# Optimization experiments

Measured on AMD Instinct MI355X. Metric: run time of the kernel, lower is better.

The kernel has to match this reference:

```python
import jax, jax.numpy as jnp
import numpy as np

B, N, I, O, H = 4, 2047, 256, 128, 4
NEG = -1e18
SLOPE = 0.2


def setup_inputs() -> dict:
    key = jax.random.key(0)
    ks = jax.random.split(key, 8)
    x = jax.random.normal(ks[0], (B, N, I), dtype=jnp.float32)
    prior_feature = jax.random.normal(ks[1], (B, O), dtype=jnp.float32)
    x_mask = jax.random.randint(ks[2], (B, N + 1), 0, 2).astype(bool)
    # learned parameters (xavier-ish scaling)
    W_lin = jax.random.normal(ks[3], (O, I), dtype=jnp.float32) * (1.0 / np.sqrt(I))
    w_head = jax.random.normal(ks[4], (H, O, O), dtype=jnp.float32) * (1.0 / np.sqrt(O))
    a_src = jax.random.normal(ks[5], (H, O), dtype=jnp.float32) * (1.0 / np.sqrt(O))
    a_dst = jax.random.normal(ks[6], (H, O), dtype=jnp.float32) * (1.0 / np.sqrt(O))
    bias = jnp.zeros((O,), dtype=jnp.float32)
    return {"x": x, "prior_feature": prior_feature, "x_mask": x_mask,
            "W_lin": W_lin, "w_head": w_head, "a_src": a_src, "a_dst": a_dst, "bias": bias}


def reference(x, prior_feature, x_mask, W_lin, w_head, a_src, a_dst, bias):
    # self_linear (no bias), then concat prior feature as extra node -> [B, N1, O]
    h = jnp.einsum('bni,oi->bno', x, W_lin)
    hp = jnp.concatenate([h, prior_feature[:, None, :]], axis=1)  # [B, N1, O]
    # per-head projection: [B,1,N1,O] @ [H,O,O] -> [B,H,N1,O]
    hp = jnp.einsum('bno,hop->bhnp', hp, w_head)
    t = jnp.tanh(hp)
    s_src = jnp.einsum('bhno,ho->bhn', t, a_src)  # [B,H,N1]
    s_dst = jnp.einsum('bhno,ho->bhn', t, a_dst)  # [B,H,N1]
    attn = s_src[..., :, None] + s_dst[..., None, :]  # [B,H,N1,N1]
    attn = jnp.where(attn >= 0, attn, SLOPE * attn)  # leaky_relu(0.2)
    mask = x_mask[:, :, None] | x_mask[:, None, :]    # [B,N1,N1]
    attn = jnp.where(mask[:, None, :, :], jnp.float32(NEG), attn)
    attn = jax.nn.softmax(attn, axis=-1)
    # dropout p=0.0 -> identity
    out = jnp.einsum('bhij,bhjo->bhio', attn, hp) + bias  # [B,H,N1,O]
    return out.mean(axis=1)  # mean over heads -> [B,N1,O]
```

## Files before the change

### kernel.cpp

```cpp
#include <hip/hip_runtime.h>
#include <hip/hip_bf16.h>
#include <cmath>


#define B_ 4
#define N_ 2047
#define N1 2048
#define I_ 256
#define O_ 128
#define H_ 4
#define NBINS 512
#define NCHUNK 4
#define CBINS (NBINS / NCHUNK)
#define STR 132
#define SLOPEC 0.2f
#define HS_STR 136
#define XS_STR 72

typedef unsigned short u16;
typedef unsigned char u8;
typedef short bf16x8 __attribute__((ext_vector_type(8)));
typedef float f32x4 __attribute__((ext_vector_type(4)));
#define MFMA16(a,b,c) __builtin_amdgcn_mfma_f32_16x16x32_bf16(a,b,c,0,0,0)

__device__ __forceinline__ float bf2f(u16 v){
  union { unsigned u; float f; } x; x.u = ((unsigned)v) << 16; return x.f;
}
__device__ __forceinline__ u16 f2bf(float f){
  union { float f; unsigned u; } x; x.f = f;
  unsigned u = x.u;
  return (u16)((u + 0x7FFFu + ((u >> 16) & 1u)) >> 16);
}
__device__ __forceinline__ float ldv(const void* p, int bf, size_t i){
  if (bf) return bf2f(reinterpret_cast<const u16*>(p)[i]);
  return reinterpret_cast<const float*>(p)[i];
}
__device__ __forceinline__ void ld8(const void* p, int bf, size_t i, float* o){
  if (bf){
    uint4 v = *reinterpret_cast<const uint4*>(reinterpret_cast<const u16*>(p) + i);
    o[0]=bf2f((u16)(v.x&0xFFFF)); o[1]=bf2f((u16)(v.x>>16));
    o[2]=bf2f((u16)(v.y&0xFFFF)); o[3]=bf2f((u16)(v.y>>16));
    o[4]=bf2f((u16)(v.z&0xFFFF)); o[5]=bf2f((u16)(v.z>>16));
    o[6]=bf2f((u16)(v.w&0xFFFF)); o[7]=bf2f((u16)(v.w>>16));
  } else {
    const float4* q = reinterpret_cast<const float4*>(reinterpret_cast<const float*>(p) + i);
    float4 a = q[0], b = q[1];
    o[0]=a.x; o[1]=a.y; o[2]=a.z; o[3]=a.w;
    o[4]=b.x; o[5]=b.y; o[6]=b.z; o[7]=b.w;
  }
}
__device__ __forceinline__ void st8bf(u16* dst, const void* src, int bf, size_t i){
  if (bf){
    *reinterpret_cast<uint4*>(dst) =
      *reinterpret_cast<const uint4*>(reinterpret_cast<const u16*>(src) + i);
  } else {
    float v[8]; ld8(src, 0, i, v);
    u16 tmp[8];
#pragma unroll
    for (int m = 0; m < 8; m++) tmp[m] = f2bf(v[m]);
    *reinterpret_cast<uint4*>(dst) = *reinterpret_cast<uint4*>(tmp);
  }
}
__device__ __forceinline__ float clS(float v){ return fminf(30.f, fmaxf(-30.f, v)); }
__device__ __forceinline__ float clH(float v){ return fminf(1e4f, fmaxf(-1e4f, v)); }
__device__ __forceinline__ int binOf(float v, float lo, float inv){
  int c = (int)((v - lo) * inv);
  c = c < 0 ? 0 : c;
  c = c > NBINS - 1 ? NBINS - 1 : c;
  return c;
}
__device__ __forceinline__ int rdmask(const u8* m, int mode, int idx){
  return mode ? (m[idx] != 0) : (((const int*)m)[idx] != 0);
}

__global__ __launch_bounds__(1024) void k0_detect(const u8* __restrict__ mask,
                                                  const void* x, const void* prior,
                                                  const void* Wlin, const void* wh,
                                                  const void* asr, const void* ads,
                                                  int* __restrict__ flags,
                                                  float* __restrict__ colsum){
  __shared__ int c[8];
  const int t = threadIdx.x;
  for (int i = t; i < B_ * H_ * O_; i += 1024) colsum[i] = 0.f;
  if (t < 8) c[t] = 0;
  __syncthreads();
  int local = 0;
  for (int i = t; i < B_ * N1; i += 1024)
    if ((i & 3) && mask[i]) local = 1;
  if (local) atomicOr(&c[0], 1);
  const void* ptrs[6] = {x, prior, Wlin, wh, asr, ads};
  const int   lens[6] = {4096, 512, 4096, 4096, 512, 512};
  for (int k = 0; k < 6; k++){
    const u16* p = (const u16*)ptrs[k];
    int g = 0;
    for (int i = t; i < lens[k]; i += 1024){
      int e = (p[i] >> 7) & 0xFF;
      if (e >= 0xC0) g++;
    }
    if (g) atomicAdd(&c[k + 1], g);
  }
  __syncthreads();
  if (t == 0) flags[0] = c[0];
  else if (t <= 6) flags[t] = (c[t] < 4) ? 1 : 0;
}

__global__ __launch_bounds__(256) void ktr(const void* __restrict__ w_head,
                                           const int* __restrict__ flags,
                                           u16* __restrict__ wT){
  const int fw = flags[4];
  const int idx = blockIdx.x * 256 + threadIdx.x;
  const int h = idx >> 14, rem = idx & 16383, p = rem >> 7, o = rem & 127;
  wT[idx] = f2bf(ldv(w_head, fw, ((size_t)h * O_ + o) * O_ + p));
}

__global__ __launch_bounds__(256) void k1_hp(const void* __restrict__ x,
                                             const void* __restrict__ prior,
                                             const void* __restrict__ Wlin,
                                             const int* __restrict__ flags,
                                             u16* __restrict__ hpb){
  __shared__ __align__(16) u16 xs[32 * XS_STR];
  __shared__ __align__(16) u16 wl[128 * XS_STR];
  const int fx = flags[1], fpf = flags[2], fw = flags[3];
  const int tile = blockIdx.x & 63;
  const int b    = blockIdx.x >> 6;
  const int n0   = tile * 32;
  const int t = threadIdx.x;
  const int w = t >> 6, lane = t & 63, m16 = lane & 15, q = lane >> 4;
  const int rbase = (w & 1) * 16;
  const int cbase = (w >> 1) * 64;
  f32x4 acc[4];
#pragma unroll
  for (int nt = 0; nt < 4; nt++) acc[nt] = (f32x4){0.f, 0.f, 0.f, 0.f};
  for (int kt = 0; kt < I_; kt += 64){
    if (kt) __syncthreads();
    {
      const int row = t >> 3, ch = t & 7;
      const int n = n0 + row;
      if (n < N_) st8bf(&xs[row * XS_STR + ch * 8], x, fx, ((size_t)b * N_ + n) * I_ + kt + ch * 8);
      else { uint4 z = make_uint4(0,0,0,0); *reinterpret_cast<uint4*>(&xs[row * XS_STR + ch * 8]) = z; }
    }
#pragma unroll
    for (int it = 0; it < 4; it++){
      const int slot = t + it * 256, row = slot >> 3, ch = slot & 7;
      st8bf(&wl[row * XS_STR + ch * 8], Wlin, fw, (size_t)row * I_ + kt + ch * 8);
    }
    __syncthreads();
#pragma unroll
    for (int ks = 0; ks < 2; ks++){
      const int k0 = ks * 32 + q * 8;
      const bf16x8 af = *reinterpret_cast<const bf16x8*>(&xs[(rbase + m16) * XS_STR + k0]);
#pragma unroll
      for (int nt = 0; nt < 4; nt++){
        const bf16x8 bfr = *reinterpret_cast<const bf16x8*>(&wl[(cbase + nt * 16 + m16) * XS_STR + k0]);
        acc[nt] = MFMA16(af, bfr, acc[nt]);
      }
    }
  }
#pragma unroll
  for (int nt = 0; nt < 4; nt++){
#pragma unroll
    for (int r = 0; r < 4; r++){
      const int n = n0 + rbase + q * 4 + r;
      const int col = cbase + nt * 16 + m16;
      const float v = (n == N_) ? ldv(prior, fpf, b * O_ + col) : acc[nt][r];
      hpb[((size_t)b * N1 + n) * O_ + col] = f2bf(v);
    }
  }
}

__global__ __launch_bounds__(256) void k2_heads(const u16* __restrict__ hpb,
                                                const u16* __restrict__ wT,
                                                const void* __restrict__ a_src,
                                                const void* __restrict__ a_dst,
                                                const int* __restrict__ flags,
                                                float* __restrict__ hph,
                                                float* __restrict__ s_src,
                                                float* __restrict__ s_dst,
                                                float* __restrict__ colsum){
  __shared__ __align__(16) u16 hsb[64 * HS_STR];
  __shared__ __align__(16) u16 wtb[128 * HS_STR];
  __shared__ float colacc[O_];
  const int fas = flags[5], fad = flags[6];
  const int tile = blockIdx.x & 31;
  const int h    = (blockIdx.x >> 5) & 3;
  const int b    = blockIdx.x >> 7;
  const int bh   = b * H_ + h;
  const int n0   = tile * 64;
  const int t = threadIdx.x;
  const int w = t >> 6, lane = t & 63, m16 = lane & 15, q = lane >> 4;
  if (t < O_) colacc[t] = 0.f;
#pragma unroll
  for (int it = 0; it < 4; it++){
    const int slot = t + it * 256, row = slot >> 4, ch = slot & 15;
    *reinterpret_cast<uint4*>(&hsb[row * HS_STR + ch * 8]) =
      *reinterpret_cast<const uint4*>(&hpb[((size_t)b * N1 + n0 + row) * O_ + ch * 8]);
  }
#pragma unroll
  for (int it = 0; it < 8; it++){
    const int slot = t + it * 256, row = slot >> 4, ch = slot & 15;
    *reinterpret_cast<uint4*>(&wtb[row * HS_STR + ch * 8]) =
      *reinterpret_cast<const uint4*>(&wT[((size_t)h * O_ + row) * O_ + ch * 8]);
  }
  __syncthreads();
  f32x4 acc[8];
#pragma unroll
  for (int nt = 0; nt < 8; nt++) acc[nt] = (f32x4){0.f, 0.f, 0.f, 0.f};
#pragma unroll
  for (int ks = 0; ks < 4; ks++){
    const int k0 = ks * 32 + q * 8;
    const bf16x8 af = *reinterpret_cast<const bf16x8*>(&hsb[(w * 16 + m16) * HS_STR + k0]);
#pragma unroll
    for (int nt = 0; nt < 8; nt++){
      const bf16x8 bfr = *reinterpret_cast<const bf16x8*>(&wtb[(nt * 16 + m16) * HS_STR + k0]);
      acc[nt] = MFMA16(af, bfr, acc[nt]);
    }
  }
  float ps[4] = {0.f, 0.f, 0.f, 0.f}, pd[4] = {0.f, 0.f, 0.f, 0.f};
#pragma unroll
  for (int nt = 0; nt < 8; nt++){
    const int col = nt * 16 + m16;
    const float asv = ldv(a_src, fas, h * O_ + col);
    const float adv = ldv(a_dst, fad, h * O_ + col);
    float colpart = 0.f;
#pragma unroll
    for (int r = 0; r < 4; r++){
      const float v = clH(acc[nt][r]);
      hph[((size_t)bh * N1 + n0 + w * 16 + q * 4 + r) * O_ + col] = v;
      colpart += v;
      const float tv = tanhf(v);
      ps[r] += tv * asv;
      pd[r] += tv * adv;
    }
    atomicAdd(&colacc[col], colpart);
  }
#pragma unroll
  for (int r = 0; r < 4; r++){
#pragma unroll
    for (int m = 8; m > 0; m >>= 1){
      ps[r] += __shfl_xor(ps[r], m);
      pd[r] += __shfl_xor(pd[r], m);
    }
    if (m16 == 0){
      const int n = n0 + w * 16 + q * 4 + r;
      s_src[(size_t)bh * N1 + n] = ps[r];
      s_dst[(size_t)bh * N1 + n] = pd[r];
    }
  }
  __syncthreads();
  if (t < O_) atomicAdd(&colsum[bh * O_ + t], colacc[t]);
}

__global__ __launch_bounds__(256) void k3a_bucket(const float* __restrict__ s_dst,
                                                  const u8* __restrict__ mask,
                                                  const int* __restrict__ flags,
                                                  float* __restrict__ sdlo,
                                                  float* __restrict__ sdinv,
                                                  int* __restrict__ binStart,
                                                  int* __restrict__ order){
  __shared__ float smn[4], smx[4];
  __shared__ float sli[2];
  __shared__ int cnt[NBINS];
  __shared__ int part[256];
  __shared__ int offs[NBINS];
  const int bh = blockIdx.x, b = bh / H_, t = threadIdx.x;
  const int md = flags[0];
  float mn = 3e38f, mx = -3e38f;
  for (int j = t; j < N1; j += 256){
    if (!rdmask(mask, md, b * N1 + j)){
      float v = clS(s_dst[(size_t)bh * N1 + j]);
      mn = fminf(mn, v); mx = fmaxf(mx, v);
    }
  }
#pragma unroll
  for (int sft = 32; sft > 0; sft >>= 1){
    mn = fminf(mn, __shfl_down(mn, sft));
    mx = fmaxf(mx, __shfl_down(mx, sft));
  }
  if ((t & 63) == 0){ smn[t >> 6] = mn; smx[t >> 6] = mx; }
  __syncthreads();
  if (t == 0){
    mn = fminf(fminf(smn[0], smn[1]), fminf(smn[2], smn[3]));
    mx = fmaxf(fmaxf(smx[0], smx[1]), fmaxf(smx[2], smx[3]));
    float range = mx - mn;
    if (!(range > 1e-30f)) range = 1.f;
    const float inv = (float)NBINS / range;
    sdlo[bh]  = mn;
    sdinv[bh] = inv;
    sli[0] = mn; sli[1] = inv;
  }
  __syncthreads();
  const float lo = sli[0], inv = sli[1];
  cnt[t] = 0; cnt[t + 256] = 0;
  __syncthreads();
  for (int j = t; j < N1; j += 256){
    if (!rdmask(mask, md, b * N1 + j))
      atomicAdd(&cnt[binOf(clS(s_dst[(size_t)bh * N1 + j]), lo, inv)], 1);
  }
  __syncthreads();
  const int s0 = cnt[2 * t], s1 = cnt[2 * t + 1];
  const int mysum = s0 + s1;
  part[t] = mysum;
  __syncthreads();
  for (int off = 1; off < 256; off <<= 1){
    int v = (t >= off) ? part[t - off] : 0;
    __syncthreads();
    part[t] += v;
    __syncthreads();
  }
  const int excl = part[t] - mysum;
  offs[2 * t] = excl;
  offs[2 * t + 1] = excl + s0;
  binStart[bh * (NBINS + 1) + 2 * t] = excl;
  binStart[bh * (NBINS + 1) + 2 * t + 1] = excl + s0;
  if (t == 255) binStart[bh * (NBINS + 1) + NBINS] = part[255];
  __syncthreads();
  for (int j = t; j < N1; j += 256){
    if (!rdmask(mask, md, b * N1 + j)){
      int bin = binOf(clS(s_dst[(size_t)bh * N1 + j]), lo, inv);
      int pos = atomicAdd(&offs[bin], 1);
      order[(size_t)bh * N1 + pos] = j;
    }
  }
}

__global__ __launch_bounds__(192) void k3b_binsum(const float* __restrict__ hph,
                                                  const float* __restrict__ s_dst,
                                                  const int* __restrict__ binStart,
                                                  const int* __restrict__ order,
                                                  float* __restrict__ binPos,
                                                  float* __restrict__ binNeg){
  __shared__ int jls[64];
  __shared__ float fpl[64], fnl[64];
  const int gb = blockIdx.x;
  const int bh = gb / NBINS, bin = gb % NBINS;
  const int t = threadIdx.x;
  const int s = binStart[bh * (NBINS + 1) + bin];
  const int e = binStart[bh * (NBINS + 1) + bin + 1];
  float ap = 0.f, an = 0.f;
  for (int mb = s; mb < e; mb += 64){
    const int cn = min(64, e - mb);
    if (t < cn){
      const int j = order[(size_t)bh * N1 + mb + t];
      const float sdj = clS(s_dst[(size_t)bh * N1 + j]);
      jls[t] = j;
      fpl[t] = __expf(sdj);
      fnl[t] = __expf(SLOPEC * sdj);
    }
    __syncthreads();
    for (int m = 0; m < cn; m++){
      const float v = (t < O_) ? hph[((size_t)bh * N1 + jls[m]) * O_ + t] : 1.f;
      ap += fpl[m] * v;
      an += fnl[m] * v;
    }
    __syncthreads();
  }
  if (t <= O_){
    const size_t basei = ((size_t)bh * NBINS + bin) * STR;
    binPos[basei + t] = ap;
    binNeg[basei + t] = an;
  }
}

__global__ __launch_bounds__(576) void k3c_scan(const float* __restrict__ binPos,
                                                const float* __restrict__ binNeg,
                                                float* __restrict__ sufPos,
                                                float* __restrict__ preNeg){
  __shared__ float csum[NCHUNK][132];
  const int blk = blockIdx.x;
  const int bh = blk & 15, arr = blk >> 4;
  const int t = threadIdx.x;
  const bool act = t < NCHUNK * 129;
  const int ch = act ? (t % 129) : 0;
  const int chunk = act ? (t / 129) : 0;
  const float* src = arr ? binPos : binNeg;
  if (act){
    float s = 0.f;
    const size_t base = ((size_t)bh * NBINS + chunk * CBINS) * STR + ch;
    for (int r = 0; r < CBINS; r++) s += src[base + (size_t)r * STR];
    csum[chunk][ch] = s;
  }
  __syncthreads();
  if (act){
    if (arr == 0){
      float acc = 0.f;
      for (int cc = 0; cc < chunk; cc++) acc += csum[cc][ch];
      for (int rr = 0; rr < CBINS; rr++){
        const int r = chunk * CBINS + rr;
        preNeg[((size_t)bh * (NBINS + 1) + r) * STR + ch] = acc;
        acc += binNeg[((size_t)bh * NBINS + r) * STR + ch];
      }
      if (chunk == NCHUNK - 1) preNeg[((size_t)bh * (NBINS + 1) + NBINS) * STR + ch] = acc;
    } else {
      float acc = 0.f;
      for (int cc = chunk + 1; cc < NCHUNK; cc++) acc += csum[cc][ch];
      for (int rr = CBINS - 1; rr >= 0; rr--){
        const int r = chunk * CBINS + rr;
        acc += binPos[((size_t)bh * NBINS + r) * STR + ch];
        sufPos[((size_t)bh * (NBINS + 1) + r) * STR + ch] = acc;
      }
      if (chunk == NCHUNK - 1) sufPos[((size_t)bh * (NBINS + 1) + NBINS) * STR + ch] = 0.f;
    }
  }
}

__global__ __launch_bounds__(512) void k3d_out(const float* __restrict__ hph,
                                               const float* __restrict__ s_src,
                                               const float* __restrict__ s_dst,
                                               const u8* __restrict__ mask,
                                               const int* __restrict__ flags,
                                               const float* __restrict__ sdlo,
                                               const float* __restrict__ sdinv,
                                               const int* __restrict__ binStart,
                                               const int* __restrict__ order,
                                               const float* __restrict__ sufPos,
                                               const float* __restrict__ preNeg,
                                               const float* __restrict__ colsum,
                                               const void* __restrict__ bias,
                                               void* __restrict__ outp){
  __shared__ float part[4 * STR];
  const int blk = blockIdx.x;
  const int b = blk >> 11, i = blk & (N1 - 1);
  const int t = threadIdx.x;
  const int h = t >> 7, o = t & 127;
  const int lane = t & 63;
  const int md = flags[0], fo = flags[1];
  const int bh = b * H_ + h;
  const int U = binStart[bh * (NBINS + 1) + NBINS];
  const bool mrow = rdmask(mask, md, b * N1 + i) != 0;
  float contrib;
  if (mrow || U == 0){
    contrib = colsum[bh * O_ + o] * (1.f / N1);
  } else {
    const float si = clS(s_src[(size_t)bh * N1 + i]);
    const float tthr = -si;
    const int c = binOf(tthr, sdlo[bh], sdinv[bh]);
    const size_t rowp = ((size_t)bh * (NBINS + 1) + c + 1) * STR;
    const size_t rown = ((size_t)bh * (NBINS + 1) + c) * STR;
    float posV = sufPos[rowp + o], posS = sufPos[rowp + O_];
    float negV = preNeg[rown + o], negS = preNeg[rown + O_];
    const int s0 = binStart[bh * (NBINS + 1) + c];
    const int e0 = binStart[bh * (NBINS + 1) + c + 1];
    for (int mb = s0; mb < e0; mb += 64){
      const int cn = min(64, e0 - mb);
      int jm = 0; float sdm = 0.f, fpm = 0.f, fnm = 0.f;
      if (lane < cn){
        jm = order[(size_t)bh * N1 + mb + lane];
        sdm = clS(s_dst[(size_t)bh * N1 + jm]);
        fpm = __expf(sdm);
        fnm = __expf(SLOPEC * sdm);
      }
      int m = 0;
      for (; m + 3 < cn; m += 4){
        const int j0 = __shfl(jm, m),     j1 = __shfl(jm, m + 1);
        const int j2 = __shfl(jm, m + 2), j3 = __shfl(jm, m + 3);
        const float hv0 = hph[((size_t)bh * N1 + j0) * O_ + o];
        const float hv1 = hph[((size_t)bh * N1 + j1) * O_ + o];
        const float hv2 = hph[((size_t)bh * N1 + j2) * O_ + o];
        const float hv3 = hph[((size_t)bh * N1 + j3) * O_ + o];
        const float sd0 = __shfl(sdm, m),     sd1 = __shfl(sdm, m + 1);
        const float sd2 = __shfl(sdm, m + 2), sd3 = __shfl(sdm, m + 3);
        const float fp0 = __shfl(fpm, m),     fp1 = __shfl(fpm, m + 1);
        const float fp2 = __shfl(fpm, m + 2), fp3 = __shfl(fpm, m + 3);
        const float fn0 = __shfl(fnm, m),     fn1 = __shfl(fnm, m + 1);
        const float fn2 = __shfl(fnm, m + 2), fn3 = __shfl(fnm, m + 3);
        if (sd0 >= tthr){ posV += fp0 * hv0; posS += fp0; } else { negV += fn0 * hv0; negS += fn0; }
        if (sd1 >= tthr){ posV += fp1 * hv1; posS += fp1; } else { negV += fn1 * hv1; negS += fn1; }
        if (sd2 >= tthr){ posV += fp2 * hv2; posS += fp2; } else { negV += fn2 * hv2; negS += fn2; }
        if (sd3 >= tthr){ posV += fp3 * hv3; posS += fp3; } else { negV += fn3 * hv3; negS += fn3; }
      }
      for (; m < cn; m++){
        const int j = __shfl(jm, m);
        const float sdj = __shfl(sdm, m);
        const float fp = __shfl(fpm, m);
        const float fn = __shfl(fnm, m);
        const float hv = hph[((size_t)bh * N1 + j) * O_ + o];
        if (sdj >= tthr){ posV += fp * hv; posS += fp; }
        else            { negV += fn * hv; negS += fn; }
      }
    }
    const float esi = __expf(si), esi2 = __expf(SLOPEC * si);
    const float den = fmaxf(esi * posS + esi2 * negS, 1e-35f);
    contrib = (esi * posV + esi2 * negV) / den;
  }
  part[h * STR + o] = contrib;
  __syncthreads();
  if (t < O_){
    const float sum = part[0 * STR + t] + part[1 * STR + t] + part[2 * STR + t] + part[3 * STR + t];
    const float v = 0.25f * sum + ldv(bias, fo, t);
    const size_t oidx = ((size_t)b * N1 + i) * O_ + t;
    if (fo) ((u16*)outp)[oidx] = f2bf(v);
    else    ((float*)outp)[oidx] = v;
  }
}

extern "C" void kernel_launch(void* const* d_in, const int* in_sizes, int n_in,
                              void* d_out, int out_size, void* d_ws, size_t ws_size,
                              hipStream_t stream){
  const void* x      = d_in[0];
  const void* prior  = d_in[1];
  const u8*   mask   = (const u8*)d_in[2];
  const void* Wlin   = d_in[3];
  const void* w_head = d_in[4];
  const void* a_src  = d_in[5];
  const void* a_dst  = d_in[6];
  const void* bias   = d_in[7];

  char* basep = (char*)d_ws;
  size_t off = 0;
  auto alloc = [&](size_t bytes) -> void* {
    off = (off + 255) & ~(size_t)255;
    void* p = basep + off;
    off += bytes;
    return p;
  };
  int*   flags    = (int*)alloc(32);
  u16*   wT       = (u16*)alloc((size_t)H_ * O_ * O_ * 2);
  u16*   hpb      = (u16*)alloc((size_t)B_ * N1 * O_ * 2);
  float* hph      = (float*)alloc((size_t)B_ * H_ * N1 * O_ * 4);
  float* s_src    = (float*)alloc((size_t)B_ * H_ * N1 * 4);
  float* s_dst    = (float*)alloc((size_t)B_ * H_ * N1 * 4);
  float* sdlo     = (float*)alloc(B_ * H_ * 4);
  float* sdinv    = (float*)alloc(B_ * H_ * 4);
  float* colsum   = (float*)alloc((size_t)B_ * H_ * O_ * 4);
  int*   binStart = (int*)alloc((size_t)B_ * H_ * (NBINS + 1) * 4);
  int*   order    = (int*)alloc((size_t)B_ * H_ * N1 * 4);
  float* binPos   = (float*)alloc((size_t)B_ * H_ * NBINS * STR * 4);
  float* binNeg   = (float*)alloc((size_t)B_ * H_ * NBINS * STR * 4);
  float* sufPos   = (float*)alloc((size_t)B_ * H_ * (NBINS + 1) * STR * 4);
  float* preNeg   = (float*)alloc((size_t)B_ * H_ * (NBINS + 1) * STR * 4);
  (void)in_sizes; (void)n_in; (void)out_size; (void)ws_size;

  hipLaunchKernelGGL(k0_detect,  dim3(1),                dim3(1024), 0, stream, mask, x, prior, Wlin, w_head, a_src, a_dst, flags, colsum);
  hipLaunchKernelGGL(ktr,        dim3(256),              dim3(256), 0, stream, w_head, flags, wT);
  hipLaunchKernelGGL(k1_hp,      dim3(B_ * 64),          dim3(256), 0, stream, x, prior, Wlin, flags, hpb);
  hipLaunchKernelGGL(k2_heads,   dim3(B_ * H_ * 32),     dim3(256), 0, stream, hpb, wT, a_src, a_dst, flags, hph, s_src, s_dst, colsum);
  hipLaunchKernelGGL(k3a_bucket, dim3(B_ * H_),          dim3(256), 0, stream, s_dst, mask, flags, sdlo, sdinv, binStart, order);
  hipLaunchKernelGGL(k3b_binsum, dim3(B_ * H_ * NBINS),  dim3(192), 0, stream, hph, s_dst, binStart, order, binPos, binNeg);
  hipLaunchKernelGGL(k3c_scan,   dim3(32),               dim3(576), 0, stream, binPos, binNeg, sufPos, preNeg);
  hipLaunchKernelGGL(k3d_out,    dim3(B_ * N1),          dim3(512), 0, stream, hph, s_src, s_dst, mask, flags, sdlo, sdinv, binStart, order, sufPos, preNeg, colsum, bias, d_out);
}
```

Before: 162.9 us.

## Aggregate pre-projection features and apply head projection after attention

Uses linearity: attention-weighted sums are taken over the shared bf16 pre-head features hpb instead of per-head projected fp32 hph, and the per-head w_head projection is applied afterward to the aggregated vector inside the output kernel. This removes the large per-head hph buffer and its writes and reads, halves gather bytes via bf16, and moves the masked-row column sums into k1. The bin count is also halved to 256, which cuts scan and binsum work but leaves more elements per bin for the exact fallback loop. It adds a 128-long dot product per output element in k3d_out.

```diff
diff --git a/kernel.cpp b/kernel.cpp
--- a/kernel.cpp
+++ b/kernel.cpp
@@ -9,7 +9,7 @@
 #define I_ 256
 #define O_ 128
 #define H_ 4
-#define NBINS 512
+#define NBINS 256
 #define NCHUNK 4
 #define CBINS (NBINS / NCHUNK)
 #define STR 132
@@ -81,7 +81,7 @@
                                                   float* __restrict__ colsum){
   __shared__ int c[8];
   const int t = threadIdx.x;
-  for (int i = t; i < B_ * H_ * O_; i += 1024) colsum[i] = 0.f;
+  for (int i = t; i < B_ * O_; i += 1024) colsum[i] = 0.f;
   if (t < 8) c[t] = 0;
   __syncthreads();
   int local = 0;
@@ -117,9 +117,11 @@
                                              const void* __restrict__ prior,
                                              const void* __restrict__ Wlin,
                                              const int* __restrict__ flags,
-                                             u16* __restrict__ hpb){
+                                             u16* __restrict__ hpb,
+                                             float* __restrict__ colsum){
   __shared__ __align__(16) u16 xs[32 * XS_STR];
   __shared__ __align__(16) u16 wl[128 * XS_STR];
+  __shared__ float colacc[O_];
   const int fx = flags[1], fpf = flags[2], fw = flags[3];
   const int tile = blockIdx.x & 63;
   const int b    = blockIdx.x >> 6;
@@ -128,6 +130,7 @@
   const int w = t >> 6, lane = t & 63, m16 = lane & 15, q = lane >> 4;
   const int rbase = (w & 1) * 16;
   const int cbase = (w >> 1) * 64;
+  if (t < O_) colacc[t] = 0.f;
   f32x4 acc[4];
 #pragma unroll
   for (int nt = 0; nt < 4; nt++) acc[nt] = (f32x4){0.f, 0.f, 0.f, 0.f};
@@ -158,14 +161,19 @@
   }
 #pragma unroll
   for (int nt = 0; nt < 4; nt++){
+    const int col = cbase + nt * 16 + m16;
+    float cp = 0.f;
 #pragma unroll
     for (int r = 0; r < 4; r++){
       const int n = n0 + rbase + q * 4 + r;
-      const int col = cbase + nt * 16 + m16;
       const float v = (n == N_) ? ldv(prior, fpf, b * O_ + col) : acc[nt][r];
       hpb[((size_t)b * N1 + n) * O_ + col] = f2bf(v);
-    }
-  }
+      cp += v;
+    }
+    atomicAdd(&colacc[col], cp);
+  }
+  __syncthreads();
+  if (t < O_) atomicAdd(&colsum[b * O_ + t], colacc[t]);
 }
 
 __global__ __launch_bounds__(256) void k2_heads(const u16* __restrict__ hpb,
@@ -173,13 +181,10 @@
                                                 const void* __restrict__ a_src,
                                                 const void* __restrict__ a_dst,
                                                 const int* __restrict__ flags,
-                                                float* __restrict__ hph,
                                                 float* __restrict__ s_src,
-                                                float* __restrict__ s_dst,
-                                                float* __restrict__ colsum){
+                                                float* __restrict__ s_dst){
   __shared__ __align__(16) u16 hsb[64 * HS_STR];
   __shared__ __align__(16) u16 wtb[128 * HS_STR];
-  __shared__ float colacc[O_];
   const int fas = flags[5], fad = flags[6];
   const int tile = blockIdx.x & 31;
   const int h    = (blockIdx.x >> 5) & 3;
@@ -188,7 +193,6 @@
   const int n0   = tile * 64;
   const int t = threadIdx.x;
   const int w = t >> 6, lane = t & 63, m16 = lane & 15, q = lane >> 4;
-  if (t < O_) colacc[t] = 0.f;
 #pragma unroll
   for (int it = 0; it < 4; it++){
     const int slot = t + it * 256, row = slot >> 4, ch = slot & 15;
@@ -221,17 +225,12 @@
     const int col = nt * 16 + m16;
     const float asv = ldv(a_src, fas, h * O_ + col);
     const float adv = ldv(a_dst, fad, h * O_ + col);
-    float colpart = 0.f;
 #pragma unroll
     for (int r = 0; r < 4; r++){
-      const float v = clH(acc[nt][r]);
-      hph[((size_t)bh * N1 + n0 + w * 16 + q * 4 + r) * O_ + col] = v;
-      colpart += v;
-      const float tv = tanhf(v);
+      const float tv = tanhf(clH(acc[nt][r]));
       ps[r] += tv * asv;
       pd[r] += tv * adv;
     }
-    atomicAdd(&colacc[col], colpart);
   }
 #pragma unroll
   for (int r = 0; r < 4; r++){
@@ -246,8 +245,6 @@
       s_dst[(size_t)bh * N1 + n] = pd[r];
     }
   }
-  __syncthreads();
-  if (t < O_) atomicAdd(&colsum[bh * O_ + t], colacc[t]);
 }
 
 __global__ __launch_bounds__(256) void k3a_bucket(const float* __restrict__ s_dst,
@@ -290,15 +287,14 @@
   }
   __syncthreads();
   const float lo = sli[0], inv = sli[1];
-  cnt[t] = 0; cnt[t + 256] = 0;
+  cnt[t] = 0;
   __syncthreads();
   for (int j = t; j < N1; j += 256){
     if (!rdmask(mask, md, b * N1 + j))
       atomicAdd(&cnt[binOf(clS(s_dst[(size_t)bh * N1 + j]), lo, inv)], 1);
   }
   __syncthreads();
-  const int s0 = cnt[2 * t], s1 = cnt[2 * t + 1];
-  const int mysum = s0 + s1;
+  const int mysum = cnt[t];
   part[t] = mysum;
   __syncthreads();
   for (int off = 1; off < 256; off <<= 1){
@@ -308,10 +304,8 @@
     __syncthreads();
   }
   const int excl = part[t] - mysum;
-  offs[2 * t] = excl;
-  offs[2 * t + 1] = excl + s0;
-  binStart[bh * (NBINS + 1) + 2 * t] = excl;
-  binStart[bh * (NBINS + 1) + 2 * t + 1] = excl + s0;
+  offs[t] = excl;
+  binStart[bh * (NBINS + 1) + t] = excl;
   if (t == 255) binStart[bh * (NBINS + 1) + NBINS] = part[255];
   __syncthreads();
   for (int j = t; j < N1; j += 256){
@@ -323,7 +317,7 @@
   }
 }
 
-__global__ __launch_bounds__(192) void k3b_binsum(const float* __restrict__ hph,
+__global__ __launch_bounds__(192) void k3b_binsum(const u16* __restrict__ hpb,
                                                   const float* __restrict__ s_dst,
                                                   const int* __restrict__ binStart,
                                                   const int* __restrict__ order,
@@ -333,6 +327,7 @@
   __shared__ float fpl[64], fnl[64];
   const int gb = blockIdx.x;
   const int bh = gb / NBINS, bin = gb % NBINS;
+  const int b  = bh / H_;
   const int t = threadIdx.x;
   const int s = binStart[bh * (NBINS + 1) + bin];
   const int e = binStart[bh * (NBINS + 1) + bin + 1];
@@ -348,7 +343,7 @@
     }
     __syncthreads();
     for (int m = 0; m < cn; m++){
-      const float v = (t < O_) ? hph[((size_t)bh * N1 + jls[m]) * O_ + t] : 1.f;
+      const float v = (t < O_) ? bf2f(hpb[((size_t)b * N1 + jls[m]) * O_ + t]) : 1.f;
       ap += fpl[m] * v;
       an += fnl[m] * v;
     }
@@ -403,7 +398,7 @@
   }
 }
 
-__global__ __launch_bounds__(512) void k3d_out(const float* __restrict__ hph,
+__global__ __launch_bounds__(512) void k3d_out(const u16* __restrict__ hpb,
                                                const float* __restrict__ s_src,
                                                const float* __restrict__ s_dst,
                                                const u8* __restrict__ mask,
@@ -415,9 +410,11 @@
                                                const float* __restrict__ sufPos,
                                                const float* __restrict__ preNeg,
                                                const float* __restrict__ colsum,
+                                               const u16* __restrict__ wT,
                                                const void* __restrict__ bias,
                                                void* __restrict__ outp){
-  __shared__ float part[4 * STR];
+  __shared__ float vsh[4 * STR];
+  __shared__ float osh[4 * STR];
   const int blk = blockIdx.x;
   const int b = blk >> 11, i = blk & (N1 - 1);
   const int t = threadIdx.x;
@@ -427,9 +424,9 @@
   const int bh = b * H_ + h;
   const int U = binStart[bh * (NBINS + 1) + NBINS];
   const bool mrow = rdmask(mask, md, b * N1 + i) != 0;
-  float contrib;
+  float vo;
   if (mrow || U == 0){
-    contrib = colsum[bh * O_ + o] * (1.f / N1);
+    vo = colsum[b * O_ + o] * (1.f / N1);
   } else {
     const float si = clS(s_src[(size_t)bh * N1 + i]);
     const float tthr = -si;
@@ -453,10 +450,10 @@
       for (; m + 3 < cn; m += 4){
         const int j0 = __shfl(jm, m),     j1 = __shfl(jm, m + 1);
         const int j2 = __shfl(jm, m + 2), j3 = __shfl(jm, m + 3);
-        const float hv0 = hph[((size_t)bh * N1 + j0) * O_ + o];
-        const float hv1 = hph[((size_t)bh * N1 + j1) * O_ + o];
-        const float hv2 = hph[((size_t)bh * N1 + j2) * O_ + o];
-        const float hv3 = hph[((size_t)bh * N1 + j3) * O_ + o];
+        const float hv0 = bf2f(hpb[((size_t)b * N1 + j0) * O_ + o]);
+        const float hv1 = bf2f(hpb[((size_t)b * N1 + j1) * O_ + o]);
+        const float hv2 = bf2f(hpb[((size_t)b * N1 + j2) * O_ + o]);
+        const float hv3 = bf2f(hpb[((size_t)b * N1 + j3) * O_ + o]);
         const float sd0 = __shfl(sdm, m),     sd1 = __shfl(sdm, m + 1);
         const float sd2 = __shfl(sdm, m + 2), sd3 = __shfl(sdm, m + 3);
         const float fp0 = __shfl(fpm, m),     fp1 = __shfl(fpm, m + 1);
@@ -473,19 +470,38 @@
         const float sdj = __shfl(sdm, m);
         const float fp = __shfl(fpm, m);
         const float fn = __shfl(fnm, m);
-        const float hv = hph[((size_t)bh * N1 + j) * O_ + o];
+        const float hv = bf2f(hpb[((size_t)b * N1 + j) * O_ + o]);
         if (sdj >= tthr){ posV += fp * hv; posS += fp; }
         else            { negV += fn * hv; negS += fn; }
       }
     }
     const float esi = __expf(si), esi2 = __expf(SLOPEC * si);
     const float den = fmaxf(esi * posS + esi2 * negS, 1e-35f);
-    contrib = (esi * posV + esi2 * negV) / den;
-  }
-  part[h * STR + o] = contrib;
+    vo = (esi * posV + esi2 * negV) / den;
+  }
+  vsh[h * STR + o] = vo;
+  __syncthreads();
+  {
+    const int p = o;
+    const u16* wrow = wT + (((size_t)h * O_ + p) << 7);
+    float dot = 0.f;
+#pragma unroll
+    for (int og = 0; og < O_; og += 8){
+      const bf16x8 wv = *reinterpret_cast<const bf16x8*>(wrow + og);
+      dot += vsh[h * STR + og + 0] * bf2f((u16)wv[0]);
+      dot += vsh[h * STR + og + 1] * bf2f((u16)wv[1]);
+      dot += vsh[h * STR + og + 2] * bf2f((u16)wv[2]);
+      dot += vsh[h * STR + og + 3] * bf2f((u16)wv[3]);
+      dot += vsh[h * STR + og + 4] * bf2f((u16)wv[4]);
+      dot += vsh[h * STR + og + 5] * bf2f((u16)wv[5]);
+      dot += vsh[h * STR + og + 6] * bf2f((u16)wv[6]);
+      dot += vsh[h * STR + og + 7] * bf2f((u16)wv[7]);
+    }
+    osh[h * STR + p] = dot;
+  }
   __syncthreads();
   if (t < O_){
-    const float sum = part[0 * STR + t] + part[1 * STR + t] + part[2 * STR + t] + part[3 * STR + t];
+    const float sum = osh[0 * STR + t] + osh[1 * STR + t] + osh[2 * STR + t] + osh[3 * STR + t];
     const float v = 0.25f * sum + ldv(bias, fo, t);
     const size_t oidx = ((size_t)b * N1 + i) * O_ + t;
     if (fo) ((u16*)outp)[oidx] = f2bf(v);
@@ -516,12 +532,11 @@
   int*   flags    = (int*)alloc(32);
   u16*   wT       = (u16*)alloc((size_t)H_ * O_ * O_ * 2);
   u16*   hpb      = (u16*)alloc((size_t)B_ * N1 * O_ * 2);
-  float* hph      = (float*)alloc((size_t)B_ * H_ * N1 * O_ * 4);
   float* s_src    = (float*)alloc((size_t)B_ * H_ * N1 * 4);
   float* s_dst    = (float*)alloc((size_t)B_ * H_ * N1 * 4);
   float* sdlo     = (float*)alloc(B_ * H_ * 4);
   float* sdinv    = (float*)alloc(B_ * H_ * 4);
-  float* colsum   = (float*)alloc((size_t)B_ * H_ * O_ * 4);
+  float* colsum   = (float*)alloc((size_t)B_ * O_ * 4);
   int*   binStart = (int*)alloc((size_t)B_ * H_ * (NBINS + 1) * 4);
   int*   order    = (int*)alloc((size_t)B_ * H_ * N1 * 4);
   float* binPos   = (float*)alloc((size_t)B_ * H_ * NBINS * STR * 4);
@@ -532,10 +547,10 @@
 
   hipLaunchKernelGGL(k0_detect,  dim3(1),                dim3(1024), 0, stream, mask, x, prior, Wlin, w_head, a_src, a_dst, flags, colsum);
   hipLaunchKernelGGL(ktr,        dim3(256),              dim3(256), 0, stream, w_head, flags, wT);
-  hipLaunchKernelGGL(k1_hp,      dim3(B_ * 64),          dim3(256), 0, stream, x, prior, Wlin, flags, hpb);
-  hipLaunchKernelGGL(k2_heads,   dim3(B_ * H_ * 32),     dim3(256), 0, stream, hpb, wT, a_src, a_dst, flags, hph, s_src, s_dst, colsum);
+  hipLaunchKernelGGL(k1_hp,      dim3(B_ * 64),          dim3(256), 0, stream, x, prior, Wlin, flags, hpb, colsum);
+  hipLaunchKernelGGL(k2_heads,   dim3(B_ * H_ * 32),     dim3(256), 0, stream, hpb, wT, a_src, a_dst, flags, s_src, s_dst);
   hipLaunchKernelGGL(k3a_bucket, dim3(B_ * H_),          dim3(256), 0, stream, s_dst, mask, flags, sdlo, sdinv, binStart, order);
-  hipLaunchKernelGGL(k3b_binsum, dim3(B_ * H_ * NBINS),  dim3(192), 0, stream, hph, s_dst, binStart, order, binPos, binNeg);
+  hipLaunchKernelGGL(k3b_binsum, dim3(B_ * H_ * NBINS),  dim3(192), 0, stream, hpb, s_dst, binStart, order, binPos, binNeg);
   hipLaunchKernelGGL(k3c_scan,   dim3(32),               dim3(576), 0, stream, binPos, binNeg, sufPos, preNeg);
-  hipLaunchKernelGGL(k3d_out,    dim3(B_ * N1),          dim3(512), 0, stream, hph, s_src, s_dst, mask, flags, sdlo, sdinv, binStart, order, sufPos, preNeg, colsum, bias, d_out);
-}
+  hipLaunchKernelGGL(k3d_out,    dim3(B_ * N1),          dim3(512), 0, stream, hpb, s_src, s_dst, mask, flags, sdlo, sdinv, binStart, order, sufPos, preNeg, colsum, wT, bias, d_out);
+}
```

After: 292.3 us. +79.5%, slower.
